# Kernel optimization log

Hardware: AMD Instinct MI355X
Metric: run time of the kernel (lower is better)

## Reference

```python
import jax, jax.numpy as jnp
import numpy as np

N, E, F, S = 20000, 160000, 16, 8
ECC1, ECC2, ECC3 = 40, 24, 24
DS = [96, 256, 768, 512, 64, 1]


def setup_inputs() -> dict:
    key = jax.random.key(0)
    ks = iter(jax.random.split(key, 40))
    inp = {}
    inp["x"] = jax.random.normal(next(ks), (N, F), dtype=jnp.float32)
    inp["edge_index"] = jax.random.randint(next(ks), (E, 2), 0, N, dtype=jnp.int32)
    inp["e"] = jax.random.uniform(next(ks), (E, S), dtype=jnp.float32)

    def dense_p(k, fi, fo):
        return (jax.random.normal(k, (fi, fo), dtype=jnp.float32) * (1.0 / np.sqrt(fi)),
                jnp.zeros((fo,), dtype=jnp.float32))

    # ECCConv params: kernel_network dense (S -> F_in*F_out), root kernel, bias
    for i, (fi, fo) in enumerate([(F, ECC1), (ECC1, ECC2), (ECC2, ECC3)], start=1):
        We, be = dense_p(next(ks), S, fi * fo)
        root, _ = dense_p(next(ks), fi, fo)
        inp[f"We{i}"], inp[f"be{i}"] = We, be
        inp[f"root{i}"], inp[f"b{i}"] = root, jnp.zeros((fo,), dtype=jnp.float32)

    dims = [ECC3] + DS
    for i in range(6):
        W, b = dense_p(next(ks), dims[i], dims[i + 1])
        inp[f"Wd{i+1}"], inp[f"bd{i+1}"] = W, b
    return inp


def _ecc(h, src, tgt, e, We, be, root, b):
    fi, fo = root.shape
    # per-edge filter matrices from edge features: [E, F_in, F_out]
    K = (e @ We + be).reshape(e.shape[0], fi, fo)
    msg = jnp.einsum('ef,efo->eo', h[src], K)          # gather + per-edge matvec
    agg = jax.ops.segment_sum(msg, tgt, num_segments=h.shape[0])  # scatter-add
    return jax.nn.relu(agg + h @ root + b)


def reference(x, edge_index, e,
              We1, be1, root1, b1,
              We2, be2, root2, b2,
              We3, be3, root3, b3,
              Wd1, bd1, Wd2, bd2, Wd3, bd3, Wd4, bd4, Wd5, bd5, Wd6, bd6):
    src, tgt = edge_index[:, 0], edge_index[:, 1]
    h = _ecc(x, src, tgt, e, We1, be1, root1, b1)
    h = _ecc(h, src, tgt, e, We2, be2, root2, b2)
    h = _ecc(h, src, tgt, e, We3, be3, root3, b3)
    g = jnp.sum(h, axis=0, keepdims=True)  # GlobalSumPool (single mode) -> [1, 24]
    for W, b in [(Wd1, bd1), (Wd2, bd2), (Wd3, bd3), (Wd4, bd4), (Wd5, bd5)]:
        g = jax.nn.relu(g @ W + b)
    return g @ Wd6 + bd6  # [1, 1]
```

## Files before the change

kernel.cpp:

```cpp
#include <hip/hip_runtime.h>

constexpr int NN  = 20000;
constexpr int NE  = 160000;
constexpr int CAP = 32;
constexpr int TN  = 32;
constexpr int NBM = 16;

__device__ inline void gstore(float* p, float v) {
    __hip_atomic_store(p, v, __ATOMIC_RELAXED, __HIP_MEMORY_SCOPE_AGENT);
}
__device__ inline float gload(const float* p) {
    return __hip_atomic_load(p, __ATOMIC_RELAXED, __HIP_MEMORY_SCOPE_AGENT);
}

__device__ inline void mbarrier(int* ctr, int target, bool wait) {
    __syncthreads();
    if (threadIdx.x == 0) {
        __threadfence();
        __hip_atomic_fetch_add(ctr, 1, __ATOMIC_ACQ_REL, __HIP_MEMORY_SCOPE_AGENT);
        if (wait)
            while (__hip_atomic_load(ctr, __ATOMIC_ACQUIRE, __HIP_MEMORY_SCOPE_AGENT) < target) {}
    }
    __syncthreads();
}

template<int FI, int FO2>
__device__ void stage_W(float* Wlds, const float* __restrict__ We,
                        const float* __restrict__ be, const float* __restrict__ root)
{
    constexpr int PW = 10 * FO2, C4 = PW / 4, O4 = FO2 / 4;
    for (int t = threadIdx.x; t < FI * C4; t += 256) {
        const int f = t / C4, r = t % C4, s = r / O4, oq = r % O4;
        const float4* src;
        if (s < 8)       src = (const float4*)(We + (size_t)s * FI * FO2 + f * FO2 + oq * 4);
        else if (s == 8) src = (const float4*)(be + f * FO2 + oq * 4);
        else             src = (const float4*)(root + f * FO2 + oq * 4);
        ((float4*)Wlds)[t] = *src;
    }
}

template<int FI, int FO2>
__device__ void gemm_tile(const float* htile, const float* Wlds,
                          const float* __restrict__ bias, float* __restrict__ Pout, int n0)
{
    constexpr int PW = 10 * FO2, C4 = PW / 4, O4 = FO2 / 4;
    constexpr int TPN = 256 / TN;
    const int nl = threadIdx.x / TPN;
    const int lane = threadIdx.x % TPN;
    const int n = n0 + nl;
    if (n >= NN) return;
    const float*  hr = &htile[nl * (FI + 4)];
    const float4* W4 = (const float4*)Wlds;
    float4* Pr = (float4*)(Pout + (size_t)n * PW);
    for (int cc = lane; cc < C4; cc += TPN) {
        float4 a = {0.f, 0.f, 0.f, 0.f};
        #pragma unroll
        for (int f = 0; f < FI; f++) {
            const float  hf = hr[f];
            const float4 w  = W4[f * C4 + cc];
            a.x = fmaf(hf, w.x, a.x); a.y = fmaf(hf, w.y, a.y);
            a.z = fmaf(hf, w.z, a.z); a.w = fmaf(hf, w.w, a.w);
        }
        if (cc >= 9 * O4) {
            const float4 b4 = ((const float4*)bias)[cc - 9 * O4];
            a.x += b4.x; a.y += b4.y; a.z += b4.z; a.w += b4.w;
        }
        Pr[cc] = a;
    }
}

__global__ __launch_bounds__(256)
void fill_nodeP1_kernel(const int* __restrict__ eidx, const float* __restrict__ e,
                        const float* __restrict__ x,
                        const float* __restrict__ We1, const float* __restrict__ be1,
                        const float* __restrict__ root1, const float* __restrict__ b1,
                        int* __restrict__ cnt, int* __restrict__ adjsrc,
                        float* __restrict__ esort, float* __restrict__ Pa)
{
    __shared__ float smem[16 * 400 + TN * 20];
    const int b = blockIdx.x, tid = threadIdx.x;
    if (b < 625) {
        const int eid = b * 256 + tid;
        const int2 st = ((const int2*)eidx)[eid];
        const int q = atomicAdd(&cnt[st.y], 1);
        if (q < CAP) {
            const int slot = st.y * CAP + q;
            adjsrc[slot] = st.x;
            const float4* e4 = (const float4*)(e + (size_t)eid * 8);
            float4* o4 = (float4*)(esort + (size_t)slot * 8);
            o4[0] = e4[0];
            o4[1] = e4[1];
        }
    } else {
        float* Wlds  = smem;
        float* htile = smem + 6400;
        stage_W<16, 40>(Wlds, We1, be1, root1);
        const int n0 = (b - 625) * TN;
        for (int t = tid; t < TN * 4; t += 256) {
            const int nl = t / 4, fq = t % 4;
            const int n = n0 + nl;
            float4 v = {0.f, 0.f, 0.f, 0.f};
            if (n < NN) v = ((const float4*)(x + (size_t)n * 16))[fq];
            *((float4*)&htile[nl * 20 + fq * 4]) = v;
        }
        __syncthreads();
        gemm_tile<16, 40>(htile, Wlds, b1, Pa, n0);
    }
}

template<int FO, int FO2>
__global__ __launch_bounds__(256)
void gather_nodeP_kernel(const float* __restrict__ Pin, const int* __restrict__ cnt,
                         const int* __restrict__ adjsrc, const float* __restrict__ esort,
                         const float* __restrict__ We2, const float* __restrict__ be2,
                         const float* __restrict__ root2, const float* __restrict__ b2,
                         float* __restrict__ Pout)
{
    constexpr int PW1 = 10 * FO;
    constexpr int OQ  = FO / 4;
    constexpr int WSZ = FO * 10 * FO2;
    __shared__ float smem[WSZ + TN * (FO + 4)];
    float* Wlds  = smem;
    float* htile = smem + WSZ;
    stage_W<FO, FO2>(Wlds, We2, be2, root2);

    const int n0 = blockIdx.x * TN;
    for (int T = threadIdx.x; T < TN * OQ; T += 256) {
        const int nl = T / OQ, oq = T % OQ;
        const int n = n0 + nl;
        float4 acc = {0.f, 0.f, 0.f, 0.f};
        if (n < NN) {
            acc = *(const float4*)(Pin + (size_t)n * PW1 + 9 * FO + oq * 4);
            const int d = min(cnt[n], CAP);
            const int*   ab    = adjsrc + n * CAP;
            const float* ebase = esort + (size_t)n * CAP * 8;
            #pragma unroll 2
            for (int j = 0; j < d; j++) {
                const int src = ab[j];
                const float* Pr = Pin + (size_t)src * PW1 + oq * 4;
                const float4 e0 = ((const float4*)(ebase + j * 8))[0];
                const float4 e1 = ((const float4*)(ebase + j * 8))[1];
                float4 a = *(const float4*)(Pr + 8 * FO);
                float4 w;
                w = *(const float4*)(Pr + 0 * FO);
                a.x = fmaf(e0.x, w.x, a.x); a.y = fmaf(e0.x, w.y, a.y);
                a.z = fmaf(e0.x, w.z, a.z); a.w = fmaf(e0.x, w.w, a.w);
                w = *(const float4*)(Pr + 1 * FO);
                a.x = fmaf(e0.y, w.x, a.x); a.y = fmaf(e0.y, w.y, a.y);
                a.z = fmaf(e0.y, w.z, a.z); a.w = fmaf(e0.y, w.w, a.w);
                w = *(const float4*)(Pr + 2 * FO);
                a.x = fmaf(e0.z, w.x, a.x); a.y = fmaf(e0.z, w.y, a.y);
                a.z = fmaf(e0.z, w.z, a.z); a.w = fmaf(e0.z, w.w, a.w);
                w = *(const float4*)(Pr + 3 * FO);
                a.x = fmaf(e0.w, w.x, a.x); a.y = fmaf(e0.w, w.y, a.y);
                a.z = fmaf(e0.w, w.z, a.z); a.w = fmaf(e0.w, w.w, a.w);
                w = *(const float4*)(Pr + 4 * FO);
                a.x = fmaf(e1.x, w.x, a.x); a.y = fmaf(e1.x, w.y, a.y);
                a.z = fmaf(e1.x, w.z, a.z); a.w = fmaf(e1.x, w.w, a.w);
                w = *(const float4*)(Pr + 5 * FO);
                a.x = fmaf(e1.y, w.x, a.x); a.y = fmaf(e1.y, w.y, a.y);
                a.z = fmaf(e1.y, w.z, a.z); a.w = fmaf(e1.y, w.w, a.w);
                w = *(const float4*)(Pr + 6 * FO);
                a.x = fmaf(e1.z, w.x, a.x); a.y = fmaf(e1.z, w.y, a.y);
                a.z = fmaf(e1.z, w.z, a.z); a.w = fmaf(e1.z, w.w, a.w);
                w = *(const float4*)(Pr + 7 * FO);
                a.x = fmaf(e1.w, w.x, a.x); a.y = fmaf(e1.w, w.y, a.y);
                a.z = fmaf(e1.w, w.z, a.z); a.w = fmaf(e1.w, w.w, a.w);
                acc.x += a.x; acc.y += a.y; acc.z += a.z; acc.w += a.w;
            }
        }
        float4 r = {fmaxf(acc.x, 0.f), fmaxf(acc.y, 0.f),
                    fmaxf(acc.z, 0.f), fmaxf(acc.w, 0.f)};
        *(float4*)&htile[nl * (FO + 4) + oq * 4] = r;
    }
    __syncthreads();
    gemm_tile<FO, FO2>(htile, Wlds, b2, Pout, n0);
}

__global__ __launch_bounds__(256)
void gather_colsum_kernel(const float* __restrict__ Pin, const int* __restrict__ cnt,
                          const int* __restrict__ adjsrc, const float* __restrict__ esort,
                          float* __restrict__ g)
{
    constexpr int FO = 24, PW1 = 240, OQ = FO / 4;
    __shared__ float gl[FO];
    const int tid = threadIdx.x;
    if (tid < FO) gl[tid] = 0.f;
    __syncthreads();

    const int n0 = blockIdx.x * TN;
    for (int T = tid; T < TN * OQ; T += 256) {
        const int nl = T / OQ, oq = T % OQ;
        const int n = n0 + nl;
        if (n >= NN) continue;
        float4 acc = *(const float4*)(Pin + (size_t)n * PW1 + 9 * FO + oq * 4);
        const int d = min(cnt[n], CAP);
        const int*   ab    = adjsrc + n * CAP;
        const float* ebase = esort + (size_t)n * CAP * 8;
        #pragma unroll 2
        for (int j = 0; j < d; j++) {
            const int src = ab[j];
            const float* Pr = Pin + (size_t)src * PW1 + oq * 4;
            const float4 e0 = ((const float4*)(ebase + j * 8))[0];
            const float4 e1 = ((const float4*)(ebase + j * 8))[1];
            float4 a = *(const float4*)(Pr + 8 * FO);
            float4 w;
            w = *(const float4*)(Pr + 0 * FO);
            a.x = fmaf(e0.x, w.x, a.x); a.y = fmaf(e0.x, w.y, a.y);
            a.z = fmaf(e0.x, w.z, a.z); a.w = fmaf(e0.x, w.w, a.w);
            w = *(const float4*)(Pr + 1 * FO);
            a.x = fmaf(e0.y, w.x, a.x); a.y = fmaf(e0.y, w.y, a.y);
            a.z = fmaf(e0.y, w.z, a.z); a.w = fmaf(e0.y, w.w, a.w);
            w = *(const float4*)(Pr + 2 * FO);
            a.x = fmaf(e0.z, w.x, a.x); a.y = fmaf(e0.z, w.y, a.y);
            a.z = fmaf(e0.z, w.z, a.z); a.w = fmaf(e0.z, w.w, a.w);
            w = *(const float4*)(Pr + 3 * FO);
            a.x = fmaf(e0.w, w.x, a.x); a.y = fmaf(e0.w, w.y, a.y);
            a.z = fmaf(e0.w, w.z, a.z); a.w = fmaf(e0.w, w.w, a.w);
            w = *(const float4*)(Pr + 4 * FO);
            a.x = fmaf(e1.x, w.x, a.x); a.y = fmaf(e1.x, w.y, a.y);
            a.z = fmaf(e1.x, w.z, a.z); a.w = fmaf(e1.x, w.w, a.w);
            w = *(const float4*)(Pr + 5 * FO);
            a.x = fmaf(e1.y, w.x, a.x); a.y = fmaf(e1.y, w.y, a.y);
            a.z = fmaf(e1.y, w.z, a.z); a.w = fmaf(e1.y, w.w, a.w);
            w = *(const float4*)(Pr + 6 * FO);
            a.x = fmaf(e1.z, w.x, a.x); a.y = fmaf(e1.z, w.y, a.y);
            a.z = fmaf(e1.z, w.z, a.z); a.w = fmaf(e1.z, w.w, a.w);
            w = *(const float4*)(Pr + 7 * FO);
            a.x = fmaf(e1.w, w.x, a.x); a.y = fmaf(e1.w, w.y, a.y);
            a.z = fmaf(e1.w, w.z, a.z); a.w = fmaf(e1.w, w.w, a.w);
            acc.x += a.x; acc.y += a.y; acc.z += a.z; acc.w += a.w;
        }
        atomicAdd(&gl[oq * 4 + 0], fmaxf(acc.x, 0.f));
        atomicAdd(&gl[oq * 4 + 1], fmaxf(acc.y, 0.f));
        atomicAdd(&gl[oq * 4 + 2], fmaxf(acc.z, 0.f));
        atomicAdd(&gl[oq * 4 + 3], fmaxf(acc.w, 0.f));
    }
    __syncthreads();
    if (tid < FO) unsafeAtomicAdd(&g[tid], gl[tid]);
}

__global__ __launch_bounds__(256)
void mlp_kernel(const float* __restrict__ g, int* __restrict__ ctr,
                const float* __restrict__ Wd1, const float* __restrict__ bd1,
                const float* __restrict__ Wd2, const float* __restrict__ bd2,
                const float* __restrict__ Wd3, const float* __restrict__ bd3,
                const float* __restrict__ Wd4, const float* __restrict__ bd4,
                const float* __restrict__ Wd5, const float* __restrict__ bd5,
                const float* __restrict__ Wd6, const float* __restrict__ bd6,
                float* __restrict__ m3, float* __restrict__ m4,
                float* __restrict__ out)
{
    __shared__ float v0[768];
    __shared__ float v1[96];
    __shared__ float red[256];
    const int tid = threadIdx.x, b = blockIdx.x;

    if (tid < 24) v0[tid] = g[tid];
    __syncthreads();
    if (tid < 96) {
        float a = bd1[tid];
        #pragma unroll
        for (int i = 0; i < 24; i++) a = fmaf(v0[i], Wd1[i * 96 + tid], a);
        v1[tid] = fmaxf(a, 0.f);
    }
    __syncthreads();

    {
        float a = bd2[tid];
        #pragma unroll
        for (int i = 0; i < 96; i++) a = fmaf(v1[i], Wd2[i * 256 + tid], a);
        red[tid] = fmaxf(a, 0.f);
    }
    __syncthreads();
    v0[tid] = red[tid];
    __syncthreads();

    if (tid < 192) {
        const int o = b * 48 + (tid % 48), kg = tid / 48;
        float a = 0.f;
        #pragma unroll 8
        for (int i = kg * 64; i < kg * 64 + 64; i++)
            a = fmaf(v0[i], Wd3[(size_t)i * 768 + o], a);
        red[tid] = a;
    }
    __syncthreads();
    if (tid < 48) {
        float s = bd3[b * 48 + tid] + red[tid] + red[48 + tid] + red[96 + tid] + red[144 + tid];
        gstore(&m3[b * 48 + tid], fmaxf(s, 0.f));
    }
    mbarrier(ctr, 1 * NBM, true);

    for (int i = tid; i < 768; i += 256) v0[i] = gload(&m3[i]);
    __syncthreads();
    {
        const int o = b * 32 + (tid & 31), kg = tid >> 5;
        float a = 0.f;
        #pragma unroll 8
        for (int i = kg * 96; i < kg * 96 + 96; i++)
            a = fmaf(v0[i], Wd4[(size_t)i * 512 + o], a);
        red[tid] = a;
    }
    __syncthreads();
    if (tid < 32) {
        float s = bd4[b * 32 + tid];
        #pragma unroll
        for (int k = 0; k < 8; k++) s += red[k * 32 + tid];
        gstore(&m4[b * 32 + tid], fmaxf(s, 0.f));
    }
    mbarrier(ctr, 2 * NBM, b == 0);

    if (b == 0) {
        for (int i = tid; i < 512; i += 256) v0[i] = gload(&m4[i]);
        __syncthreads();
        {
            const int o = tid & 63, kg = tid >> 6;
            float a = 0.f;
            #pragma unroll 8
            for (int i = kg * 128; i < kg * 128 + 128; i++)
                a = fmaf(v0[i], Wd5[(size_t)i * 64 + o], a);
            red[tid] = a;
        }
        __syncthreads();
        if (tid < 64) {
            float s = bd5[tid] + red[tid] + red[64 + tid] + red[128 + tid] + red[192 + tid];
            float v = fmaxf(s, 0.f) * Wd6[tid];
            #pragma unroll
            for (int off = 32; off > 0; off >>= 1)
                v += __shfl_down(v, off, 64);
            if (tid == 0) out[0] = v + bd6[0];
        }
    }
}

extern "C" void kernel_launch(void* const* d_in, const int* in_sizes, int n_in,
                              void* d_out, int out_size, void* d_ws, size_t ws_size,
                              hipStream_t stream)
{
    const float* x     = (const float*)d_in[0];
    const int*   eidx  = (const int*)  d_in[1];
    const float* e     = (const float*)d_in[2];
    const float* We1   = (const float*)d_in[3];  const float* be1 = (const float*)d_in[4];
    const float* root1 = (const float*)d_in[5];  const float* b1  = (const float*)d_in[6];
    const float* We2   = (const float*)d_in[7];  const float* be2 = (const float*)d_in[8];
    const float* root2 = (const float*)d_in[9];  const float* b2  = (const float*)d_in[10];
    const float* We3   = (const float*)d_in[11]; const float* be3 = (const float*)d_in[12];
    const float* root3 = (const float*)d_in[13]; const float* b3  = (const float*)d_in[14];
    const float* Wd1 = (const float*)d_in[15]; const float* bd1 = (const float*)d_in[16];
    const float* Wd2 = (const float*)d_in[17]; const float* bd2 = (const float*)d_in[18];
    const float* Wd3 = (const float*)d_in[19]; const float* bd3 = (const float*)d_in[20];
    const float* Wd4 = (const float*)d_in[21]; const float* bd4 = (const float*)d_in[22];
    const float* Wd5 = (const float*)d_in[23]; const float* bd5 = (const float*)d_in[24];
    const float* Wd6 = (const float*)d_in[25]; const float* bd6 = (const float*)d_in[26];

    int*   wi     = (int*)d_ws;
    int*   cnt    = wi;
    float* g      = (float*)d_ws + 20000;
    int*   mctr   = wi + 20032;
    float* m3     = (float*)d_ws + 20064;
    float* m4     = m3 + 768;
    int*   adjsrc = wi + 21760;
    float* wf     = (float*)d_ws;
    float* esort  = wf + 661760;
    float* Pa     = wf + 5781760;
    float* Pb     = wf + 13781760;

    hipMemsetAsync(d_ws, 0, (size_t)21760 * sizeof(int), stream);

    fill_nodeP1_kernel<<<1250, 256, 0, stream>>>(eidx, e, x, We1, be1, root1, b1,
                                                 cnt, adjsrc, esort, Pa);

    gather_nodeP_kernel<40, 24><<<625, 256, 0, stream>>>(Pa, cnt, adjsrc, esort,
                                                         We2, be2, root2, b2, Pb);

    gather_nodeP_kernel<24, 24><<<625, 256, 0, stream>>>(Pb, cnt, adjsrc, esort,
                                                         We3, be3, root3, b3, Pa);

    gather_colsum_kernel<<<625, 256, 0, stream>>>(Pa, cnt, adjsrc, esort, g);

    mlp_kernel<<<NBM, 256, 0, stream>>>(g, mctr,
                                        Wd1, bd1, Wd2, bd2, Wd3, bd3,
                                        Wd4, bd4, Wd5, bd5, Wd6, bd6,
                                        m3, m4, (float*)d_out);
}
```

Before: 271.7 us.

## Split neighbor gather across threads and halve LDS weight staging

The gather kernels now use 8-node tiles (2500 blocks) and split each node's neighbor list across J threads per output quad, combining partial sums with LDS atomics before applying ReLU. The per-layer weight matrix is staged into LDS in two halves, and the node GEMM runs in two passes, which cuts LDS use and allows an occupancy hint of 6 blocks. The goal is more parallelism and better latency hiding on the irregular gather. The cost is that weights are restaged once per 8 nodes instead of once per 32, plus extra syncs and LDS atomics.

```diff
diff --git a/kernel.cpp b/kernel.cpp
--- a/kernel.cpp
+++ b/kernel.cpp
@@ -36,6 +36,23 @@
         else if (s == 8) src = (const float4*)(be + f * FO2 + oq * 4);
         else             src = (const float4*)(root + f * FO2 + oq * 4);
         ((float4*)Wlds)[t] = *src;
+    }
+}
+
+template<int FI, int FO2, int CH>
+__device__ void stage_half(float* Wh, const float* __restrict__ We,
+                           const float* __restrict__ be, const float* __restrict__ root,
+                           int c0)
+{
+    constexpr int O4 = FO2 / 4;
+    for (int t = threadIdx.x; t < FI * CH; t += 256) {
+        const int f = t / CH, ccp = t % CH, cc = c0 + ccp;
+        const int s = cc / O4, oq = cc % O4;
+        const float4* src;
+        if (s < 8)       src = (const float4*)(We + (size_t)s * FI * FO2 + f * FO2 + oq * 4);
+        else if (s == 8) src = (const float4*)(be + f * FO2 + oq * 4);
+        else             src = (const float4*)(root + f * FO2 + oq * 4);
+        ((float4*)Wh)[t] = *src;
     }
 }
 
@@ -69,6 +86,72 @@
     }
 }
 
+template<int FI, int FO2, int TN2>
+__device__ void gemm_half(const float* htile, const float* Wh,
+                          const float* __restrict__ bias, float* __restrict__ Pout,
+                          int n0, int c0)
+{
+    constexpr int PW = 10 * FO2, C4 = PW / 4, CH = C4 / 2, O4 = FO2 / 4;
+    constexpr int TPN = 256 / TN2;
+    constexpr int HS  = FI + 4;
+    const int nl = threadIdx.x / TPN, lane = threadIdx.x % TPN;
+    const int n = n0 + nl;
+    const float*  hr = &htile[nl * HS];
+    const float4* W4 = (const float4*)Wh;
+    float4* Pr = (float4*)(Pout + (size_t)n * PW);
+    for (int ccp = lane; ccp < CH; ccp += TPN) {
+        const int cc = c0 + ccp;
+        float4 a = {0.f, 0.f, 0.f, 0.f};
+        #pragma unroll
+        for (int f = 0; f < FI; f++) {
+            const float  hf = hr[f];
+            const float4 w  = W4[f * CH + ccp];
+            a.x = fmaf(hf, w.x, a.x); a.y = fmaf(hf, w.y, a.y);
+            a.z = fmaf(hf, w.z, a.z); a.w = fmaf(hf, w.w, a.w);
+        }
+        if (cc >= 9 * O4) {
+            const float4 b4 = ((const float4*)bias)[cc - 9 * O4];
+            a.x += b4.x; a.y += b4.y; a.z += b4.z; a.w += b4.w;
+        }
+        Pr[cc] = a;
+    }
+}
+
+template<int FO>
+__device__ inline void edge_fma(float4& acc, const float* __restrict__ Pr,
+                                const float* __restrict__ eq)
+{
+    const float4 e0 = ((const float4*)eq)[0];
+    const float4 e1 = ((const float4*)eq)[1];
+    float4 a = *(const float4*)(Pr + 8 * FO);
+    float4 w;
+    w = *(const float4*)(Pr + 0 * FO);
+    a.x = fmaf(e0.x, w.x, a.x); a.y = fmaf(e0.x, w.y, a.y);
+    a.z = fmaf(e0.x, w.z, a.z); a.w = fmaf(e0.x, w.w, a.w);
+    w = *(const float4*)(Pr + 1 * FO);
+    a.x = fmaf(e0.y, w.x, a.x); a.y = fmaf(e0.y, w.y, a.y);
+    a.z = fmaf(e0.y, w.z, a.z); a.w = fmaf(e0.y, w.w, a.w);
+    w = *(const float4*)(Pr + 2 * FO);
+    a.x = fmaf(e0.z, w.x, a.x); a.y = fmaf(e0.z, w.y, a.y);
+    a.z = fmaf(e0.z, w.z, a.z); a.w = fmaf(e0.z, w.w, a.w);
+    w = *(const float4*)(Pr + 3 * FO);
+    a.x = fmaf(e0.w, w.x, a.x); a.y = fmaf(e0.w, w.y, a.y);
+    a.z = fmaf(e0.w, w.z, a.z); a.w = fmaf(e0.w, w.w, a.w);
+    w = *(const float4*)(Pr + 4 * FO);
+    a.x = fmaf(e1.x, w.x, a.x); a.y = fmaf(e1.x, w.y, a.y);
+    a.z = fmaf(e1.x, w.z, a.z); a.w = fmaf(e1.x, w.w, a.w);
+    w = *(const float4*)(Pr + 5 * FO);
+    a.x = fmaf(e1.y, w.x, a.x); a.y = fmaf(e1.y, w.y, a.y);
+    a.z = fmaf(e1.y, w.z, a.z); a.w = fmaf(e1.y, w.w, a.w);
+    w = *(const float4*)(Pr + 6 * FO);
+    a.x = fmaf(e1.z, w.x, a.x); a.y = fmaf(e1.z, w.y, a.y);
+    a.z = fmaf(e1.z, w.z, a.z); a.w = fmaf(e1.z, w.w, a.w);
+    w = *(const float4*)(Pr + 7 * FO);
+    a.x = fmaf(e1.w, w.x, a.x); a.y = fmaf(e1.w, w.y, a.y);
+    a.z = fmaf(e1.w, w.z, a.z); a.w = fmaf(e1.w, w.w, a.w);
+    acc.x += a.x; acc.y += a.y; acc.z += a.z; acc.w += a.w;
+}
+
 __global__ __launch_bounds__(256)
 void fill_nodeP1_kernel(const int* __restrict__ eidx, const float* __restrict__ e,
                         const float* __restrict__ x,
@@ -108,133 +191,116 @@
     }
 }
 
-template<int FO, int FO2>
-__global__ __launch_bounds__(256)
-void gather_nodeP_kernel(const float* __restrict__ Pin, const int* __restrict__ cnt,
-                         const int* __restrict__ adjsrc, const float* __restrict__ esort,
-                         const float* __restrict__ We2, const float* __restrict__ be2,
-                         const float* __restrict__ root2, const float* __restrict__ b2,
-                         float* __restrict__ Pout)
+template<int FO, int FO2, int TN2, int J>
+__global__ __launch_bounds__(256, 6)
+void gather_nodeP2_kernel(const float* __restrict__ Pin, const int* __restrict__ cnt,
+                          const int* __restrict__ adjsrc, const float* __restrict__ esort,
+                          const float* __restrict__ We2, const float* __restrict__ be2,
+                          const float* __restrict__ root2, const float* __restrict__ b2,
+                          float* __restrict__ Pout)
 {
     constexpr int PW1 = 10 * FO;
+    constexpr int PW2 = 10 * FO2;
+    constexpr int C4  = PW2 / 4;
+    constexpr int CH  = C4 / 2;
     constexpr int OQ  = FO / 4;
-    constexpr int WSZ = FO * 10 * FO2;
-    __shared__ float smem[WSZ + TN * (FO + 4)];
-    float* Wlds  = smem;
-    float* htile = smem + WSZ;
-    stage_W<FO, FO2>(Wlds, We2, be2, root2);
-
-    const int n0 = blockIdx.x * TN;
-    for (int T = threadIdx.x; T < TN * OQ; T += 256) {
-        const int nl = T / OQ, oq = T % OQ;
+    constexpr int HS  = FO + 4;
+    __shared__ float Wh[FO * CH * 4];
+    __shared__ float htile[TN2 * HS];
+    const int tid = threadIdx.x;
+    const int n0  = blockIdx.x * TN2;
+
+    stage_half<FO, FO2, CH>(Wh, We2, be2, root2, 0);
+    for (int t = tid; t < TN2 * OQ; t += 256) {
+        const int nl = t / OQ, oq = t % OQ;
+        *(float4*)&htile[nl * HS + oq * 4] =
+            *(const float4*)(Pin + (size_t)(n0 + nl) * PW1 + 9 * FO + oq * 4);
+    }
+    __syncthreads();
+
+    for (int T = tid; T < TN2 * OQ * J; T += 256) {
+        const int nl = T / (OQ * J), r = T % (OQ * J), oq = r / J, jh = r % J;
         const int n = n0 + nl;
+        const int d = min(cnt[n], CAP);
+        if (jh >= d) continue;
         float4 acc = {0.f, 0.f, 0.f, 0.f};
-        if (n < NN) {
-            acc = *(const float4*)(Pin + (size_t)n * PW1 + 9 * FO + oq * 4);
-            const int d = min(cnt[n], CAP);
-            const int*   ab    = adjsrc + n * CAP;
-            const float* ebase = esort + (size_t)n * CAP * 8;
-            #pragma unroll 2
-            for (int j = 0; j < d; j++) {
-                const int src = ab[j];
-                const float* Pr = Pin + (size_t)src * PW1 + oq * 4;
-                const float4 e0 = ((const float4*)(ebase + j * 8))[0];
-                const float4 e1 = ((const float4*)(ebase + j * 8))[1];
-                float4 a = *(const float4*)(Pr + 8 * FO);
-                float4 w;
-                w = *(const float4*)(Pr + 0 * FO);
-                a.x = fmaf(e0.x, w.x, a.x); a.y = fmaf(e0.x, w.y, a.y);
-                a.z = fmaf(e0.x, w.z, a.z); a.w = fmaf(e0.x, w.w, a.w);
-                w = *(const float4*)(Pr + 1 * FO);
-                a.x = fmaf(e0.y, w.x, a.x); a.y = fmaf(e0.y, w.y, a.y);
-                a.z = fmaf(e0.y, w.z, a.z); a.w = fmaf(e0.y, w.w, a.w);
-                w = *(const float4*)(Pr + 2 * FO);
-                a.x = fmaf(e0.z, w.x, a.x); a.y = fmaf(e0.z, w.y, a.y);
-                a.z = fmaf(e0.z, w.z, a.z); a.w = fmaf(e0.z, w.w, a.w);
-                w = *(const float4*)(Pr + 3 * FO);
-                a.x = fmaf(e0.w, w.x, a.x); a.y = fmaf(e0.w, w.y, a.y);
-                a.z = fmaf(e0.w, w.z, a.z); a.w = fmaf(e0.w, w.w, a.w);
-                w = *(const float4*)(Pr + 4 * FO);
-                a.x = fmaf(e1.x, w.x, a.x); a.y = fmaf(e1.x, w.y, a.y);
-                a.z = fmaf(e1.x, w.z, a.z); a.w = fmaf(e1.x, w.w, a.w);
-                w = *(const float4*)(Pr + 5 * FO);
-                a.x = fmaf(e1.y, w.x, a.x); a.y = fmaf(e1.y, w.y, a.y);
-                a.z = fmaf(e1.y, w.z, a.z); a.w = fmaf(e1.y, w.w, a.w);
-                w = *(const float4*)(Pr + 6 * FO);
-                a.x = fmaf(e1.z, w.x, a.x); a.y = fmaf(e1.z, w.y, a.y);
-                a.z = fmaf(e1.z, w.z, a.z); a.w = fmaf(e1.z, w.w, a.w);
-                w = *(const float4*)(Pr + 7 * FO);
-                a.x = fmaf(e1.w, w.x, a.x); a.y = fmaf(e1.w, w.y, a.y);
-                a.z = fmaf(e1.w, w.z, a.z); a.w = fmaf(e1.w, w.w, a.w);
-                acc.x += a.x; acc.y += a.y; acc.z += a.z; acc.w += a.w;
-            }
-        }
-        float4 r = {fmaxf(acc.x, 0.f), fmaxf(acc.y, 0.f),
-                    fmaxf(acc.z, 0.f), fmaxf(acc.w, 0.f)};
-        *(float4*)&htile[nl * (FO + 4) + oq * 4] = r;
-    }
-    __syncthreads();
-    gemm_tile<FO, FO2>(htile, Wlds, b2, Pout, n0);
-}
-
-__global__ __launch_bounds__(256)
-void gather_colsum_kernel(const float* __restrict__ Pin, const int* __restrict__ cnt,
-                          const int* __restrict__ adjsrc, const float* __restrict__ esort,
-                          float* __restrict__ g)
-{
-    constexpr int FO = 24, PW1 = 240, OQ = FO / 4;
+        const int*   ab    = adjsrc + n * CAP;
+        const float* ebase = esort + (size_t)n * CAP * 8;
+        for (int j = jh; j < d; j += J) {
+            const int src = ab[j];
+            edge_fma<FO>(acc, Pin + (size_t)src * PW1 + oq * 4, ebase + j * 8);
+        }
+        float* hp = &htile[nl * HS + oq * 4];
+        atomicAdd(hp + 0, acc.x);
+        atomicAdd(hp + 1, acc.y);
+        atomicAdd(hp + 2, acc.z);
+        atomicAdd(hp + 3, acc.w);
+    }
+    __syncthreads();
+
+    for (int t = tid; t < TN2 * OQ; t += 256) {
+        float4* p = (float4*)&htile[(t / OQ) * HS + (t % OQ) * 4];
+        float4 v = *p;
+        v.x = fmaxf(v.x, 0.f); v.y = fmaxf(v.y, 0.f);
+        v.z = fmaxf(v.z, 0.f); v.w = fmaxf(v.w, 0.f);
+        *p = v;
+    }
+    __syncthreads();
+
+    gemm_half<FO, FO2, TN2>(htile, Wh, b2, Pout, n0, 0);
+    __syncthreads();
+    stage_half<FO, FO2, CH>(Wh, We2, be2, root2, CH);
+    __syncthreads();
+    gemm_half<FO, FO2, TN2>(htile, Wh, b2, Pout, n0, CH);
+}
+
+template<int TN2, int J>
+__global__ __launch_bounds__(256, 6)
+void gather_colsum2_kernel(const float* __restrict__ Pin, const int* __restrict__ cnt,
+                           const int* __restrict__ adjsrc, const float* __restrict__ esort,
+                           float* __restrict__ g)
+{
+    constexpr int FO = 24, PW1 = 240, OQ = 6, HS = 28;
+    __shared__ float htile[TN2 * HS];
     __shared__ float gl[FO];
     const int tid = threadIdx.x;
+    const int n0  = blockIdx.x * TN2;
+
     if (tid < FO) gl[tid] = 0.f;
-    __syncthreads();
-
-    const int n0 = blockIdx.x * TN;
-    for (int T = tid; T < TN * OQ; T += 256) {
-        const int nl = T / OQ, oq = T % OQ;
+    for (int t = tid; t < TN2 * OQ; t += 256) {
+        const int nl = t / OQ, oq = t % OQ;
+        *(float4*)&htile[nl * HS + oq * 4] =
+            *(const float4*)(Pin + (size_t)(n0 + nl) * PW1 + 9 * FO + oq * 4);
+    }
+    __syncthreads();
+
+    for (int T = tid; T < TN2 * OQ * J; T += 256) {
+        const int nl = T / (OQ * J), r = T % (OQ * J), oq = r / J, jh = r % J;
         const int n = n0 + nl;
-        if (n >= NN) continue;
-        float4 acc = *(const float4*)(Pin + (size_t)n * PW1 + 9 * FO + oq * 4);
         const int d = min(cnt[n], CAP);
+        if (jh >= d) continue;
+        float4 acc = {0.f, 0.f, 0.f, 0.f};
         const int*   ab    = adjsrc + n * CAP;
         const float* ebase = esort + (size_t)n * CAP * 8;
-        #pragma unroll 2
-        for (int j = 0; j < d; j++) {
+        for (int j = jh; j < d; j += J) {
             const int src = ab[j];
-            const float* Pr = Pin + (size_t)src * PW1 + oq * 4;
-            const float4 e0 = ((const float4*)(ebase + j * 8))[0];
-            const float4 e1 = ((const float4*)(ebase + j * 8))[1];
-            float4 a = *(const float4*)(Pr + 8 * FO);
-            float4 w;
-            w = *(const float4*)(Pr + 0 * FO);
-            a.x = fmaf(e0.x, w.x, a.x); a.y = fmaf(e0.x, w.y, a.y);
-            a.z = fmaf(e0.x, w.z, a.z); a.w = fmaf(e0.x, w.w, a.w);
-            w = *(const float4*)(Pr + 1 * FO);
-            a.x = fmaf(e0.y, w.x, a.x); a.y = fmaf(e0.y, w.y, a.y);
-            a.z = fmaf(e0.y, w.z, a.z); a.w = fmaf(e0.y, w.w, a.w);
-            w = *(const float4*)(Pr + 2 * FO);
-            a.x = fmaf(e0.z, w.x, a.x); a.y = fmaf(e0.z, w.y, a.y);
-            a.z = fmaf(e0.z, w.z, a.z); a.w = fmaf(e0.z, w.w, a.w);
-            w = *(const float4*)(Pr + 3 * FO);
-            a.x = fmaf(e0.w, w.x, a.x); a.y = fmaf(e0.w, w.y, a.y);
-            a.z = fmaf(e0.w, w.z, a.z); a.w = fmaf(e0.w, w.w, a.w);
-            w = *(const float4*)(Pr + 4 * FO);
-            a.x = fmaf(e1.x, w.x, a.x); a.y = fmaf(e1.x, w.y, a.y);
-            a.z = fmaf(e1.x, w.z, a.z); a.w = fmaf(e1.x, w.w, a.w);
-            w = *(const float4*)(Pr + 5 * FO);
-            a.x = fmaf(e1.y, w.x, a.x); a.y = fmaf(e1.y, w.y, a.y);
-            a.z = fmaf(e1.y, w.z, a.z); a.w = fmaf(e1.y, w.w, a.w);
-            w = *(const float4*)(Pr + 6 * FO);
-            a.x = fmaf(e1.z, w.x, a.x); a.y = fmaf(e1.z, w.y, a.y);
-            a.z = fmaf(e1.z, w.z, a.z); a.w = fmaf(e1.z, w.w, a.w);
-            w = *(const float4*)(Pr + 7 * FO);
-            a.x = fmaf(e1.w, w.x, a.x); a.y = fmaf(e1.w, w.y, a.y);
-            a.z = fmaf(e1.w, w.z, a.z); a.w = fmaf(e1.w, w.w, a.w);
-            acc.x += a.x; acc.y += a.y; acc.z += a.z; acc.w += a.w;
-        }
-        atomicAdd(&gl[oq * 4 + 0], fmaxf(acc.x, 0.f));
-        atomicAdd(&gl[oq * 4 + 1], fmaxf(acc.y, 0.f));
-        atomicAdd(&gl[oq * 4 + 2], fmaxf(acc.z, 0.f));
-        atomicAdd(&gl[oq * 4 + 3], fmaxf(acc.w, 0.f));
+            edge_fma<FO>(acc, Pin + (size_t)src * PW1 + oq * 4, ebase + j * 8);
+        }
+        float* hp = &htile[nl * HS + oq * 4];
+        atomicAdd(hp + 0, acc.x);
+        atomicAdd(hp + 1, acc.y);
+        atomicAdd(hp + 2, acc.z);
+        atomicAdd(hp + 3, acc.w);
+    }
+    __syncthreads();
+
+    for (int t = tid; t < TN2 * OQ; t += 256) {
+        const int nl = t / OQ, oq = t % OQ;
+        const float4 v = *(const float4*)&htile[nl * HS + oq * 4];
+        atomicAdd(&gl[oq * 4 + 0], fmaxf(v.x, 0.f));
+        atomicAdd(&gl[oq * 4 + 1], fmaxf(v.y, 0.f));
+        atomicAdd(&gl[oq * 4 + 2], fmaxf(v.z, 0.f));
+        atomicAdd(&gl[oq * 4 + 3], fmaxf(v.w, 0.f));
     }
     __syncthreads();
     if (tid < FO) unsafeAtomicAdd(&g[tid], gl[tid]);
@@ -370,13 +436,13 @@
     fill_nodeP1_kernel<<<1250, 256, 0, stream>>>(eidx, e, x, We1, be1, root1, b1,
                                                  cnt, adjsrc, esort, Pa);
 
-    gather_nodeP_kernel<40, 24><<<625, 256, 0, stream>>>(Pa, cnt, adjsrc, esort,
-                                                         We2, be2, root2, b2, Pb);
-
-    gather_nodeP_kernel<24, 24><<<625, 256, 0, stream>>>(Pb, cnt, adjsrc, esort,
-                                                         We3, be3, root3, b3, Pa);
-
-    gather_colsum_kernel<<<625, 256, 0, stream>>>(Pa, cnt, adjsrc, esort, g);
+    gather_nodeP2_kernel<40, 24, 8, 4><<<2500, 256, 0, stream>>>(Pa, cnt, adjsrc, esort,
+                                                                 We2, be2, root2, b2, Pb);
+
+    gather_nodeP2_kernel<24, 24, 8, 6><<<2500, 256, 0, stream>>>(Pb, cnt, adjsrc, esort,
+                                                                 We3, be3, root3, b3, Pa);
+
+    gather_colsum2_kernel<8, 6><<<2500, 256, 0, stream>>>(Pa, cnt, adjsrc, esort, g);
 
     mlp_kernel<<<NBM, 256, 0, stream>>>(g, mctr,
                                         Wd1, bd1, Wd2, bd2, Wd3, bd3,
```

Result: slower. 305.3 us (+12.4%).

## Replace pull-based gather with source-bucketed push and atomic scatter-add

Applied to the files above, without the earlier changes.

Edges are now bucketed by source node instead of target, so each source keeps its nine projected filter rows in registers and pushes a message per outgoing edge to its target with a global float atomic add. The per-layer work is split into a push kernel and a separate node GEMM kernel, and the final colsum is a flat reduction. This removes the repeated random reads of source rows per edge, but adds many global atomics, extra kernel launches, a larger memset, and nondeterministic summation order. Sorted edge features are no longer copied; edges are read by id from the original array.

```diff
diff --git a/kernel.cpp b/kernel.cpp
--- a/kernel.cpp
+++ b/kernel.cpp
@@ -70,26 +70,21 @@
 }
 
 __global__ __launch_bounds__(256)
-void fill_nodeP1_kernel(const int* __restrict__ eidx, const float* __restrict__ e,
-                        const float* __restrict__ x,
+void fill_nodeP1_kernel(const int* __restrict__ eidx, const float* __restrict__ x,
                         const float* __restrict__ We1, const float* __restrict__ be1,
                         const float* __restrict__ root1, const float* __restrict__ b1,
-                        int* __restrict__ cnt, int* __restrict__ adjsrc,
-                        float* __restrict__ esort, float* __restrict__ Pa)
+                        int* __restrict__ cnt_s, int* __restrict__ se_eid,
+                        int* __restrict__ se_tgt, float* __restrict__ Pa)
 {
     __shared__ float smem[16 * 400 + TN * 20];
     const int b = blockIdx.x, tid = threadIdx.x;
     if (b < 625) {
         const int eid = b * 256 + tid;
         const int2 st = ((const int2*)eidx)[eid];
-        const int q = atomicAdd(&cnt[st.y], 1);
+        const int q = atomicAdd(&cnt_s[st.x], 1);
         if (q < CAP) {
-            const int slot = st.y * CAP + q;
-            adjsrc[slot] = st.x;
-            const float4* e4 = (const float4*)(e + (size_t)eid * 8);
-            float4* o4 = (float4*)(esort + (size_t)slot * 8);
-            o4[0] = e4[0];
-            o4[1] = e4[1];
+            se_eid[st.x * CAP + q] = eid;
+            se_tgt[st.x * CAP + q] = st.y;
         }
     } else {
         float* Wlds  = smem;
@@ -108,136 +103,83 @@
     }
 }
 
-template<int FO, int FO2>
-__global__ __launch_bounds__(256)
-void gather_nodeP_kernel(const float* __restrict__ Pin, const int* __restrict__ cnt,
-                         const int* __restrict__ adjsrc, const float* __restrict__ esort,
-                         const float* __restrict__ We2, const float* __restrict__ be2,
-                         const float* __restrict__ root2, const float* __restrict__ b2,
-                         float* __restrict__ Pout)
-{
-    constexpr int PW1 = 10 * FO;
-    constexpr int OQ  = FO / 4;
-    constexpr int WSZ = FO * 10 * FO2;
-    __shared__ float smem[WSZ + TN * (FO + 4)];
+template<int FO, int PW1, int GSZ>
+__global__ __launch_bounds__(256)
+void push_kernel(const float* __restrict__ Pin, const int* __restrict__ cnt_s,
+                 const int* __restrict__ se_eid, const int* __restrict__ se_tgt,
+                 const float* __restrict__ e, float* __restrict__ hagg)
+{
+    constexpr int SPB = 256 / GSZ;
+    const int tid = threadIdx.x;
+    const int o   = tid % GSZ;
+    const int n   = blockIdx.x * SPB + tid / GSZ;
+
+    float p[9];
+    if (o < FO) {
+        #pragma unroll
+        for (int s = 0; s < 9; s++)
+            p[s] = Pin[(size_t)n * PW1 + s * FO + o];
+    }
+    const int d = min(cnt_s[n], CAP);
+    const int* eb = se_eid + n * CAP;
+    const int* tb = se_tgt + n * CAP;
+    for (int j = 0; j < d; j++) {
+        const int eid = eb[j];
+        const int tgt = tb[j];
+        const float4 e0 = *(const float4*)(e + (size_t)eid * 8);
+        const float4 e1 = *(const float4*)(e + (size_t)eid * 8 + 4);
+        if (o < FO) {
+            float m = p[8];
+            m = fmaf(e0.x, p[0], m); m = fmaf(e0.y, p[1], m);
+            m = fmaf(e0.z, p[2], m); m = fmaf(e0.w, p[3], m);
+            m = fmaf(e1.x, p[4], m); m = fmaf(e1.y, p[5], m);
+            m = fmaf(e1.z, p[6], m); m = fmaf(e1.w, p[7], m);
+            unsafeAtomicAdd(&hagg[(size_t)tgt * FO + o], m);
+        }
+    }
+}
+
+template<int FI, int FO2>
+__global__ __launch_bounds__(256)
+void hgemm_kernel(const float* __restrict__ hagg, const float* __restrict__ Pin,
+                  const float* __restrict__ We, const float* __restrict__ be,
+                  const float* __restrict__ root, const float* __restrict__ bias,
+                  float* __restrict__ Pout)
+{
+    constexpr int PW_IN = 10 * FI, HS = FI + 4, OQ = FI / 4;
+    __shared__ float smem[FI * 10 * FO2 + TN * HS];
     float* Wlds  = smem;
-    float* htile = smem + WSZ;
-    stage_W<FO, FO2>(Wlds, We2, be2, root2);
-
+    float* htile = smem + FI * 10 * FO2;
+    stage_W<FI, FO2>(Wlds, We, be, root);
     const int n0 = blockIdx.x * TN;
-    for (int T = threadIdx.x; T < TN * OQ; T += 256) {
-        const int nl = T / OQ, oq = T % OQ;
+    for (int t = threadIdx.x; t < TN * OQ; t += 256) {
+        const int nl = t / OQ, oq = t % OQ;
         const int n = n0 + nl;
-        float4 acc = {0.f, 0.f, 0.f, 0.f};
-        if (n < NN) {
-            acc = *(const float4*)(Pin + (size_t)n * PW1 + 9 * FO + oq * 4);
-            const int d = min(cnt[n], CAP);
-            const int*   ab    = adjsrc + n * CAP;
-            const float* ebase = esort + (size_t)n * CAP * 8;
-            #pragma unroll 2
-            for (int j = 0; j < d; j++) {
-                const int src = ab[j];
-                const float* Pr = Pin + (size_t)src * PW1 + oq * 4;
-                const float4 e0 = ((const float4*)(ebase + j * 8))[0];
-                const float4 e1 = ((const float4*)(ebase + j * 8))[1];
-                float4 a = *(const float4*)(Pr + 8 * FO);
-                float4 w;
-                w = *(const float4*)(Pr + 0 * FO);
-                a.x = fmaf(e0.x, w.x, a.x); a.y = fmaf(e0.x, w.y, a.y);
-                a.z = fmaf(e0.x, w.z, a.z); a.w = fmaf(e0.x, w.w, a.w);
-                w = *(const float4*)(Pr + 1 * FO);
-                a.x = fmaf(e0.y, w.x, a.x); a.y = fmaf(e0.y, w.y, a.y);
-                a.z = fmaf(e0.y, w.z, a.z); a.w = fmaf(e0.y, w.w, a.w);
-                w = *(const float4*)(Pr + 2 * FO);
-                a.x = fmaf(e0.z, w.x, a.x); a.y = fmaf(e0.z, w.y, a.y);
-                a.z = fmaf(e0.z, w.z, a.z); a.w = fmaf(e0.z, w.w, a.w);
-                w = *(const float4*)(Pr + 3 * FO);
-                a.x = fmaf(e0.w, w.x, a.x); a.y = fmaf(e0.w, w.y, a.y);
-                a.z = fmaf(e0.w, w.z, a.z); a.w = fmaf(e0.w, w.w, a.w);
-                w = *(const float4*)(Pr + 4 * FO);
-                a.x = fmaf(e1.x, w.x, a.x); a.y = fmaf(e1.x, w.y, a.y);
-                a.z = fmaf(e1.x, w.z, a.z); a.w = fmaf(e1.x, w.w, a.w);
-                w = *(const float4*)(Pr + 5 * FO);
-                a.x = fmaf(e1.y, w.x, a.x); a.y = fmaf(e1.y, w.y, a.y);
-                a.z = fmaf(e1.y, w.z, a.z); a.w = fmaf(e1.y, w.w, a.w);
-                w = *(const float4*)(Pr + 6 * FO);
-                a.x = fmaf(e1.z, w.x, a.x); a.y = fmaf(e1.z, w.y, a.y);
-                a.z = fmaf(e1.z, w.z, a.z); a.w = fmaf(e1.z, w.w, a.w);
-                w = *(const float4*)(Pr + 7 * FO);
-                a.x = fmaf(e1.w, w.x, a.x); a.y = fmaf(e1.w, w.y, a.y);
-                a.z = fmaf(e1.w, w.z, a.z); a.w = fmaf(e1.w, w.w, a.w);
-                acc.x += a.x; acc.y += a.y; acc.z += a.z; acc.w += a.w;
-            }
-        }
-        float4 r = {fmaxf(acc.x, 0.f), fmaxf(acc.y, 0.f),
-                    fmaxf(acc.z, 0.f), fmaxf(acc.w, 0.f)};
-        *(float4*)&htile[nl * (FO + 4) + oq * 4] = r;
-    }
-    __syncthreads();
-    gemm_tile<FO, FO2>(htile, Wlds, b2, Pout, n0);
-}
-
-__global__ __launch_bounds__(256)
-void gather_colsum_kernel(const float* __restrict__ Pin, const int* __restrict__ cnt,
-                          const int* __restrict__ adjsrc, const float* __restrict__ esort,
-                          float* __restrict__ g)
-{
-    constexpr int FO = 24, PW1 = 240, OQ = FO / 4;
-    __shared__ float gl[FO];
+        const float4 hv = *(const float4*)(hagg + (size_t)n * FI + oq * 4);
+        const float4 rv = *(const float4*)(Pin + (size_t)n * PW_IN + 9 * FI + oq * 4);
+        float4 r = {fmaxf(hv.x + rv.x, 0.f), fmaxf(hv.y + rv.y, 0.f),
+                    fmaxf(hv.z + rv.z, 0.f), fmaxf(hv.w + rv.w, 0.f)};
+        *(float4*)&htile[nl * HS + oq * 4] = r;
+    }
+    __syncthreads();
+    gemm_tile<FI, FO2>(htile, Wlds, bias, Pout, n0);
+}
+
+__global__ __launch_bounds__(256)
+void colsum_kernel(const float* __restrict__ hagg3, const float* __restrict__ Pin,
+                   float* __restrict__ g)
+{
+    __shared__ float gl[24];
     const int tid = threadIdx.x;
-    if (tid < FO) gl[tid] = 0.f;
-    __syncthreads();
-
-    const int n0 = blockIdx.x * TN;
-    for (int T = tid; T < TN * OQ; T += 256) {
-        const int nl = T / OQ, oq = T % OQ;
-        const int n = n0 + nl;
-        if (n >= NN) continue;
-        float4 acc = *(const float4*)(Pin + (size_t)n * PW1 + 9 * FO + oq * 4);
-        const int d = min(cnt[n], CAP);
-        const int*   ab    = adjsrc + n * CAP;
-        const float* ebase = esort + (size_t)n * CAP * 8;
-        #pragma unroll 2
-        for (int j = 0; j < d; j++) {
-            const int src = ab[j];
-            const float* Pr = Pin + (size_t)src * PW1 + oq * 4;
-            const float4 e0 = ((const float4*)(ebase + j * 8))[0];
-            const float4 e1 = ((const float4*)(ebase + j * 8))[1];
-            float4 a = *(const float4*)(Pr + 8 * FO);
-            float4 w;
-            w = *(const float4*)(Pr + 0 * FO);
-            a.x = fmaf(e0.x, w.x, a.x); a.y = fmaf(e0.x, w.y, a.y);
-            a.z = fmaf(e0.x, w.z, a.z); a.w = fmaf(e0.x, w.w, a.w);
-            w = *(const float4*)(Pr + 1 * FO);
-            a.x = fmaf(e0.y, w.x, a.x); a.y = fmaf(e0.y, w.y, a.y);
-            a.z = fmaf(e0.y, w.z, a.z); a.w = fmaf(e0.y, w.w, a.w);
-            w = *(const float4*)(Pr + 2 * FO);
-            a.x = fmaf(e0.z, w.x, a.x); a.y = fmaf(e0.z, w.y, a.y);
-            a.z = fmaf(e0.z, w.z, a.z); a.w = fmaf(e0.z, w.w, a.w);
-            w = *(const float4*)(Pr + 3 * FO);
-            a.x = fmaf(e0.w, w.x, a.x); a.y = fmaf(e0.w, w.y, a.y);
-            a.z = fmaf(e0.w, w.z, a.z); a.w = fmaf(e0.w, w.w, a.w);
-            w = *(const float4*)(Pr + 4 * FO);
-            a.x = fmaf(e1.x, w.x, a.x); a.y = fmaf(e1.x, w.y, a.y);
-            a.z = fmaf(e1.x, w.z, a.z); a.w = fmaf(e1.x, w.w, a.w);
-            w = *(const float4*)(Pr + 5 * FO);
-            a.x = fmaf(e1.y, w.x, a.x); a.y = fmaf(e1.y, w.y, a.y);
-            a.z = fmaf(e1.y, w.z, a.z); a.w = fmaf(e1.y, w.w, a.w);
-            w = *(const float4*)(Pr + 6 * FO);
-            a.x = fmaf(e1.z, w.x, a.x); a.y = fmaf(e1.z, w.y, a.y);
-            a.z = fmaf(e1.z, w.z, a.z); a.w = fmaf(e1.z, w.w, a.w);
-            w = *(const float4*)(Pr + 7 * FO);
-            a.x = fmaf(e1.w, w.x, a.x); a.y = fmaf(e1.w, w.y, a.y);
-            a.z = fmaf(e1.w, w.z, a.z); a.w = fmaf(e1.w, w.w, a.w);
-            acc.x += a.x; acc.y += a.y; acc.z += a.z; acc.w += a.w;
-        }
-        atomicAdd(&gl[oq * 4 + 0], fmaxf(acc.x, 0.f));
-        atomicAdd(&gl[oq * 4 + 1], fmaxf(acc.y, 0.f));
-        atomicAdd(&gl[oq * 4 + 2], fmaxf(acc.z, 0.f));
-        atomicAdd(&gl[oq * 4 + 3], fmaxf(acc.w, 0.f));
-    }
-    __syncthreads();
-    if (tid < FO) unsafeAtomicAdd(&g[tid], gl[tid]);
+    if (tid < 24) gl[tid] = 0.f;
+    __syncthreads();
+    for (int i = blockIdx.x * 256 + tid; i < NN * 24; i += gridDim.x * 256) {
+        const int n = i / 24, o = i - n * 24;
+        const float v = fmaxf(hagg3[i] + Pin[(size_t)n * 240 + 216 + o], 0.f);
+        atomicAdd(&gl[o], v);
+    }
+    __syncthreads();
+    if (tid < 24) unsafeAtomicAdd(&g[tid], gl[tid]);
 }
 
 __global__ __launch_bounds__(256)
@@ -354,29 +296,36 @@
     const float* Wd6 = (const float*)d_in[25]; const float* bd6 = (const float*)d_in[26];
 
     int*   wi     = (int*)d_ws;
-    int*   cnt    = wi;
-    float* g      = (float*)d_ws + 20000;
+    float* wf     = (float*)d_ws;
+    int*   cnt_s  = wi;
+    float* g      = wf + 20000;
     int*   mctr   = wi + 20032;
-    float* m3     = (float*)d_ws + 20064;
+    float* m3     = wf + 20064;
     float* m4     = m3 + 768;
-    int*   adjsrc = wi + 21760;
-    float* wf     = (float*)d_ws;
-    float* esort  = wf + 661760;
-    float* Pa     = wf + 5781760;
-    float* Pb     = wf + 13781760;
-
-    hipMemsetAsync(d_ws, 0, (size_t)21760 * sizeof(int), stream);
-
-    fill_nodeP1_kernel<<<1250, 256, 0, stream>>>(eidx, e, x, We1, be1, root1, b1,
-                                                 cnt, adjsrc, esort, Pa);
-
-    gather_nodeP_kernel<40, 24><<<625, 256, 0, stream>>>(Pa, cnt, adjsrc, esort,
-                                                         We2, be2, root2, b2, Pb);
-
-    gather_nodeP_kernel<24, 24><<<625, 256, 0, stream>>>(Pb, cnt, adjsrc, esort,
-                                                         We3, be3, root3, b3, Pa);
-
-    gather_colsum_kernel<<<625, 256, 0, stream>>>(Pa, cnt, adjsrc, esort, g);
+    float* hagg1  = wf + 21344;
+    float* hagg2  = wf + 821344;
+    float* hagg3  = wf + 1301344;
+    int*   se_eid = wi + 1781344;
+    int*   se_tgt = wi + 2421344;
+    float* Pa     = wf + 3061344;
+    float* Pb     = wf + 11061344;
+
+    hipMemsetAsync(d_ws, 0, (size_t)1781344 * sizeof(float), stream);
+
+    fill_nodeP1_kernel<<<1250, 256, 0, stream>>>(eidx, x, We1, be1, root1, b1,
+                                                 cnt_s, se_eid, se_tgt, Pa);
+
+    push_kernel<40, 400, 64><<<NN / 4, 256, 0, stream>>>(Pa, cnt_s, se_eid, se_tgt, e, hagg1);
+
+    hgemm_kernel<40, 24><<<625, 256, 0, stream>>>(hagg1, Pa, We2, be2, root2, b2, Pb);
+
+    push_kernel<24, 240, 32><<<NN / 8, 256, 0, stream>>>(Pb, cnt_s, se_eid, se_tgt, e, hagg2);
+
+    hgemm_kernel<24, 24><<<625, 256, 0, stream>>>(hagg2, Pb, We3, be3, root3, b3, Pa);
+
+    push_kernel<24, 240, 32><<<NN / 8, 256, 0, stream>>>(Pa, cnt_s, se_eid, se_tgt, e, hagg3);
+
+    colsum_kernel<<<128, 256, 0, stream>>>(hagg3, Pa, g);
 
     mlp_kernel<<<NBM, 256, 0, stream>>>(g, mctr,
                                         Wd1, bd1, Wd2, bd2, Wd3, bd3,
```

Result: slower. 282.0 us (+3.8%).
